# Performance work log

Hardware: AMD Instinct MI355X
Metric: run time of the kernel (lower is better)

The kernel has to match this reference:

```python
import jax, jax.numpy as jnp
import numpy as np

FIR_LO = {
    'db4': np.array([-0.0105974017850021, 0.0328830116668852, 0.0308413818355607, -0.1870348117188811,
                     -0.0279837694169839, 0.6308807679295904, 0.7148465705529155, 0.2303778133088964], np.float32),
    'db6': np.array([0.00107730108499558, -0.00477725751101065, -0.0005538422009938, 0.03158203931748603,
                     0.02752286553030533, -0.0975016055873225, -0.12976686756709563, 0.22626469396544,
                     0.3152503517092432, -0.7511339080210959, 0.4946238903984534, 0.1115407433501095], np.float32),
    'sym6': np.array([-0.007800708325034148, 0.001767711864242804, 0.04472490177066578, -0.02106029251230056,
                      -0.0726375227866, 0.3379294217282401, 0.787641141030194, 0.4910559419267466,
                      -0.048311742585632, -0.1179901111484105, 0.00349071208421747, 0.01540410932702737], np.float32),
    'coif5': np.array([-3.459977283621256e-05, -7.098330313814114e-05, 0.0004662169601128863, 0.001117518770890601,
                       -0.002574517688750223, -0.00900797613666158, 0.015880544863615904, 0.03455502757306163,
                       -0.08230192710688598, -0.07179982161931202, 0.42848347637761874, 0.7937772226256206,
                       0.4051769024096169, -0.06112339000267287, -0.06577191128185562, 0.023452696141836267,
                       0.007782596427325418, -0.003793512864491014, -0.0002606761356811993, 0.000107502882505652,
                       1.10319778524429e-05, -5.520763127949e-06, -1.0682196848076e-06, 5.236425333584e-07,
                       1.125098976034e-07, -5.417490769329e-08, -8.8631e-09, 4.2921e-09, 6.7e-10, -3.2e-10], np.float32),
}

CANDIDATES = ['db4', 'db6', 'sym6', 'coif5', 'bior53', 'bior97']
LIFT_53 = [(-0.5, True), (0.25, False)]
LIFT_97 = [(-1.586134342, True), (-0.05298011854, False), (0.8829110762, True), (0.4435068522, False)]


def _pad_reflect(x, hpad, wpad):
    if hpad == (0, 0) and wpad == (0, 0):
        return x
    return jnp.pad(x, ((0, 0), (0, 0), hpad, wpad), mode='reflect')


def _lo(name):
    lo = jnp.asarray(FIR_LO[name])
    return lo / (jnp.sqrt(jnp.sum(lo * lo)) + 1e-12)


def _hi_from_lo(lo):
    L = lo.shape[0]
    sign = jnp.cos(jnp.pi * jnp.arange(L, dtype=lo.dtype))  # (-1)^n
    return sign * lo[::-1]


def _sep_conv(x, k, dim):
    # x: (N,1,H,W); k: (L,) 1D filter applied separably along dim (cross-correlation, stride 1)
    L = k.shape[0]
    pl = (L - 1) // 2
    pa, pb = ((pl - 1, pl) if L % 2 == 0 else (pl, pl))
    if dim == 'W':
        xp = _pad_reflect(x, (0, 0), (pa, pb))
        kern = k.reshape(1, 1, 1, L)
    else:
        xp = _pad_reflect(x, (pa, pb), (0, 0))
        kern = k.reshape(1, 1, L, 1)
    return jax.lax.conv_general_dilated(xp, kern, (1, 1), 'VALID',
                                        dimension_numbers=('NCHW', 'OIHW', 'NCHW'))


def _split_even_odd(x, dim):
    if dim == 'W':
        if x.shape[3] % 2 == 1:
            x = _pad_reflect(x, (0, 0), (0, 1))
        return x[..., 0::2], x[..., 1::2]
    if x.shape[2] % 2 == 1:
        x = _pad_reflect(x, (0, 1), (0, 0))
    return x[..., 0::2, :], x[..., 1::2, :]


def _nb_sum(x, dim):
    # 0.5*(left+right) with reflect padding == conv with kernel [0.5, 0, 0.5]
    if dim == 'W':
        xp = _pad_reflect(x, (0, 0), (1, 1))
        return 0.5 * (xp[..., :-2] + xp[..., 2:])
    xp = _pad_reflect(x, (1, 1), (0, 0))
    return 0.5 * (xp[..., :-2, :] + xp[..., 2:, :])


def _lift(x, dim, steps, sA, sD):
    even, odd = _split_even_odd(x, dim)
    for coeff, is_pred in steps:
        if is_pred:
            odd = odd + coeff * _nb_sum(even, dim)
        else:
            even = even + coeff * _nb_sum(odd, dim)
    return sA * even, sD * odd


def _one_level_1d(x, cand, dim, p):
    if cand == 'bior53':
        return _lift(x, dim, LIFT_53, p['s53A'], p['s53D'])
    if cand == 'bior97':
        return _lift(x, dim, LIFT_97, p['s97A'], p['s97D'])
    lo = _lo(cand)
    return _sep_conv(x, lo, dim), _sep_conv(x, _hi_from_lo(lo), dim)


def _one_level_2d(x, cand, p):
    H, W = x.shape[2], x.shape[3]
    Lw, Hw = _one_level_1d(x, cand, 'W', p)
    LL, LH = _one_level_1d(Lw, cand, 'H', p)
    HL, HH = _one_level_1d(Hw, cand, 'H', p)

    def up(t):
        if t.shape[2] == H and t.shape[3] == W:
            return t
        return jax.image.resize(t, (t.shape[0], t.shape[1], H, W), method='bilinear')  # align_corners=False

    hf = p['hf']
    return up(LL), up(LH) * hf, up(HL) * hf, up(HH) * hf


def reference(x, gate_w1, gate_b1, gate_w2, gate_b2, scale53_A, scale53_D,
              scale97_A, scale97_D, hf_scale, proj_w, proj_b):
    B, C, H, W = x.shape
    # gate: 1x1 conv -> relu -> 1x1 conv -> softmax over K candidates
    h = jax.nn.relu(jnp.einsum('bchw,oc->bohw', x, gate_w1) + gate_b1[None, :, None, None])
    logits = jnp.einsum('bchw,oc->bohw', h, gate_w2) + gate_b2[None, :, None, None]
    gate_w = jax.nn.softmax(logits, axis=1)  # (B,K,H,W)

    x_bc = x.reshape(B * C, 1, H, W)
    p = {'s53A': scale53_A, 's53D': scale53_D, 's97A': scale97_A, 's97D': scale97_D, 'hf': hf_scale}
    bands = [_one_level_2d(x_bc, c, p) for c in CANDIDATES]
    # stack over K candidates -> (B*C, K, H, W) per subband
    LL = jnp.concatenate([b[0] for b in bands], axis=1)
    LH = jnp.concatenate([b[1] for b in bands], axis=1)
    HL = jnp.concatenate([b[2] for b in bands], axis=1)
    HH = jnp.concatenate([b[3] for b in bands], axis=1)

    w = jnp.repeat(gate_w, C, axis=0)  # (B*C,K,H,W), same as repeat_interleave on batch
    w = w / (jnp.sum(w, axis=1, keepdims=True) + 1e-12)
    LL_f = jnp.sum(LL * w, axis=1)
    LH_f = jnp.sum(LH * w, axis=1)
    HL_f = jnp.sum(HL * w, axis=1)
    HH_f = jnp.sum(HH * w, axis=1)

    Y = jnp.stack([LL_f, LH_f, HL_f, HH_f], axis=1).reshape(B, C * 4, H, W)
    return jnp.einsum('bchw,oc->bohw', Y, proj_w) + proj_b[None, :, None, None]


def setup_inputs() -> dict:
    key = jax.random.key(0)
    ks = jax.random.split(key, 5)
    C, hidden, K, Cout = 32, 8, 6, 32
    return {
        'x': jax.random.normal(ks[0], (4, C, 192, 192), jnp.float32),
        'gate_w1': jax.random.normal(ks[1], (hidden, C), jnp.float32) * (1.0 / np.sqrt(C)),
        'gate_b1': jnp.zeros((hidden,), jnp.float32),
        'gate_w2': jax.random.normal(ks[2], (K, hidden), jnp.float32) * (1.0 / np.sqrt(hidden)),
        'gate_b2': jnp.zeros((K,), jnp.float32),
        'scale53_A': jnp.float32(1.0),
        'scale53_D': jnp.float32(1.0),
        'scale97_A': jnp.float32(1.149604398),
        'scale97_D': jnp.float32(1.0 / 1.149604398),
        'hf_scale': jnp.float32(0.9),
        'proj_w': jax.random.normal(ks[3], (Cout, 4 * C), jnp.float32) * (1.0 / np.sqrt(4 * C)),
        'proj_b': jnp.zeros((Cout,), jnp.float32),
    }
```

## Files before the change

### kernel.cpp

```cpp
#include <hip/hip_runtime.h>
#include <hip/hip_fp16.h>

#define HW 36864
#define IMGS 128

typedef _Float16 h16;
typedef _Float16 v8h __attribute__((ext_vector_type(8)));
typedef _Float16 v4h __attribute__((ext_vector_type(4)));
typedef _Float16 v2h __attribute__((ext_vector_type(2)));
typedef float v4f __attribute__((ext_vector_type(4)));

static __device__ __forceinline__ int imax(int a, int b) { return a > b ? a : b; }
static __device__ __forceinline__ int imin(int a, int b) { return a < b ? a : b; }

__device__ __constant__ float LIFT_C[6] = {
  -0.5f, 0.25f,
  -1.586134342f, -0.05298011854f, 0.8829110762f, 0.4435068522f
};
__device__ __constant__ int FIR_L[4]   = {8, 12, 12, 30};
__device__ __constant__ int FIR_PA[4]  = {2, 4, 4, 13};
__device__ __constant__ int FIR_OFF[4] = {0, 8, 20, 32};

__device__ constexpr float FIRC[62] = {
  -0.0105974017850021f, 0.0328830116668852f, 0.0308413818355607f, -0.1870348117188811f,
  -0.0279837694169839f, 0.6308807679295904f, 0.7148465705529155f, 0.2303778133088964f,
  0.00107730108499558f, -0.00477725751101065f, -0.0005538422009938f, 0.03158203931748603f,
  0.02752286553030533f, -0.0975016055873225f, -0.12976686756709563f, 0.22626469396544f,
  0.3152503517092432f, -0.7511339080210959f, 0.4946238903984534f, 0.1115407433501095f,
  -0.007800708325034148f, 0.001767711864242804f, 0.04472490177066578f, -0.02106029251230056f,
  -0.0726375227866f, 0.3379294217282401f, 0.787641141030194f, 0.4910559419267466f,
  -0.048311742585632f, -0.1179901111484105f, 0.00349071208421747f, 0.01540410932702737f,
  -3.459977283621256e-05f, -7.098330313814114e-05f, 0.0004662169601128863f, 0.001117518770890601f,
  -0.002574517688750223f, -0.00900797613666158f, 0.015880544863615904f, 0.03455502757306163f,
  -0.08230192710688598f, -0.07179982161931202f, 0.42848347637761874f, 0.7937772226256206f,
  0.4051769024096169f, -0.06112339000267287f, -0.06577191128185562f, 0.023452696141836267f,
  0.007782596427325418f, -0.003793512864491014f, -0.0002606761356811993f, 0.000107502882505652f,
  1.10319778524429e-05f, -5.520763127949e-06f, -1.0682196848076e-06f, 5.236425333584e-07f,
  1.125098976034e-07f, -5.417490769329e-08f, -8.8631e-09f, 4.2921e-09f, 6.7e-10f, -3.2e-10f,
};

__global__ __launch_bounds__(256) void k_gate(
    const float* __restrict__ x, const float* __restrict__ w1, const float* __restrict__ b1,
    const float* __restrict__ w2, const float* __restrict__ b2, h16* __restrict__ gate)
{
  __shared__ float w1s[256], b1s[8], w2s[48], b2s[6];
  int tid = threadIdx.x;
  w1s[tid] = w1[tid];
  if (tid < 8)  b1s[tid] = b1[tid];
  if (tid < 48) w2s[tid] = w2[tid];
  if (tid < 6)  b2s[tid] = b2[tid];
  __syncthreads();
  int px = blockIdx.x * 256 + tid;
  int b = px / HW, p = px - b * HW;
  const float* xb = x + (size_t)b * 32 * HW + p;
  float xv[32];
#pragma unroll
  for (int c = 0; c < 32; ++c) xv[c] = xb[(size_t)c * HW];
  float hb[8];
#pragma unroll
  for (int j = 0; j < 8; ++j) {
    float s = b1s[j];
#pragma unroll
    for (int c = 0; c < 32; ++c) s += w1s[j * 32 + c] * xv[c];
    hb[j] = fmaxf(s, 0.f);
  }
  float e[6], mx = -1e30f;
#pragma unroll
  for (int k = 0; k < 6; ++k) {
    float s = b2s[k];
#pragma unroll
    for (int j = 0; j < 8; ++j) s += w2s[k * 8 + j] * hb[j];
    e[k] = s; mx = fmaxf(mx, s);
  }
  float se = 0.f;
#pragma unroll
  for (int k = 0; k < 6; ++k) { e[k] = expf(e[k] - mx); se += e[k]; }
  float inv = 1.f / se, s2 = 0.f;
#pragma unroll
  for (int k = 0; k < 6; ++k) { e[k] *= inv; s2 += e[k]; }
  float inv2 = 1.f / (s2 + 1e-12f);
  h16* gp = gate + (size_t)b * 6 * HW + p;
#pragma unroll
  for (int k = 0; k < 6; ++k) gp[(size_t)k * HW] = (h16)(e[k] * inv2);
}

__global__ __launch_bounds__(64) void k_build(
    h16* __restrict__ Kall, const float* __restrict__ s53A, const float* __restrict__ s53D,
    const float* __restrict__ s97A, const float* __restrict__ s97D)
{
  const int col = blockIdx.x;
  const int mat = blockIdx.y;
  const int cand = mat >> 1, side = mat & 1;
  const int tid = threadIdx.x;
  h16* out = Kall + (size_t)mat * HW;
  if (cand < 4) {
    const int Lf = FIR_L[cand], PA = FIR_PA[cand], OFF = FIR_OFF[cand];
    float ss = 0.f;
    for (int j = 0; j < Lf; ++j) ss += FIRC[OFF + j] * FIRC[OFF + j];
    const float invn = 1.f / (sqrtf(ss) + 1e-12f);
    for (int i = tid; i < 192; i += 64) {
      const int d = (i < 96) ? 1 : 2;
      const int q0 = i - d;
      const int i0 = imax(q0, 0), i1 = imin(q0 + 1, 189);
      const float tt = (float)d - (float)(2 * i + 1) * (1.f / 192.f);
      float c0 = 0.f, c1 = 0.f;
      for (int j = 0; j < Lf; ++j) {
        float fj = side ? (((j & 1) ? -1.f : 1.f) * FIRC[OFF + Lf - 1 - j]) : FIRC[OFF + j];
        fj *= invn;
        int r0 = i0 + j - PA; r0 = r0 < 0 ? -r0 : (r0 > 191 ? 382 - r0 : r0);
        int r1 = i1 + j - PA; r1 = r1 < 0 ? -r1 : (r1 > 191 ? 382 - r1 : r1);
        if (r0 == col) c0 += fj;
        if (r1 == col) c1 += fj;
      }
      out[(size_t)i * 192 + col] = (h16)((1.f - tt) * c0 + tt * c1);
    }
  } else {
    __shared__ float yb[192];
    __shared__ float sb[96];
    yb[tid] = 0.f; yb[tid + 64] = 0.f; yb[tid + 128] = 0.f;
    __syncthreads();
    if (tid == 0) yb[col] = 1.f;
    __syncthreads();
    const int c97 = (cand == 5);
    const int base = c97 ? 2 : 0, ns = c97 ? 4 : 2;
    for (int s = 0; s < ns; ++s) {
      const float cf = LIFT_C[base + s] * 0.5f;
      for (int j = tid; j < 96; j += 64) {
        int jm = (j == 0) ? 1 : j - 1, jp = (j == 95) ? 94 : j + 1;
        if ((s & 1) == 0) yb[2 * j + 1] += cf * (yb[2 * jm] + yb[2 * jp]);
        else              yb[2 * j]     += cf * (yb[2 * jm + 1] + yb[2 * jp + 1]);
      }
      __syncthreads();
    }
    const float sA = c97 ? s97A[0] : s53A[0];
    const float sD = c97 ? s97D[0] : s53D[0];
    for (int u = tid; u < 96; u += 64)
      sb[u] = side ? sD * yb[2 * u + 1] : sA * yb[2 * u];
    __syncthreads();
    for (int i = tid; i < 192; i += 64) {
      const int u0 = (i >> 1) + (i & 1) - 1;
      const float tt = (i & 1) ? 0.25f : 0.75f;
      const int a0 = imax(u0, 0), a1 = imin(u0 + 1, 95);
      out[(size_t)i * 192 + col] = (h16)((1.f - tt) * sb[a0] + tt * sb[a1]);
    }
  }
}

__global__ __launch_bounds__(768) void k_gw(
    const float* __restrict__ x, const h16* __restrict__ Kall, h16* __restrict__ P)
{
  __shared__ h16 As[96 * 200];
  const int half = blockIdx.x;
  const int img  = blockIdx.y;
  const int tid = threadIdx.x;
  const float* xi = x + (size_t)img * HW + (size_t)half * 96 * 192;
  for (int u = tid; u < 2304; u += 768) {
    int r = u / 24, c8 = u - r * 24;
    float4 v0 = *(const float4*)(xi + (size_t)r * 192 + c8 * 8);
    float4 v1 = *(const float4*)(xi + (size_t)r * 192 + c8 * 8 + 4);
    v8h h;
    h[0] = (h16)v0.x; h[1] = (h16)v0.y; h[2] = (h16)v0.z; h[3] = (h16)v0.w;
    h[4] = (h16)v1.x; h[5] = (h16)v1.y; h[6] = (h16)v1.z; h[7] = (h16)v1.w;
    *(v8h*)(As + (size_t)r * 200 + c8 * 8) = h;
  }
  __syncthreads();
  const int lane = tid & 63, wv = tid >> 6;
  const int lm = lane & 15, quad = lane >> 4;
  const int mt = wv >> 1, nh = wv & 1;
  const int mrow = mt * 16;
  const int hg = half * 96 + mrow + quad * 4;
  for (int plane = 0; plane < 12; ++plane) {
    const h16* KB = Kall + (size_t)plane * HW;
    h16* Pp = P + ((size_t)plane * IMGS + img) * HW;
    for (int t6 = 0; t6 < 6; ++t6) {
      const int nt = nh * 6 + t6;
      const int n0 = nt * 16;
      const int ktlo = imax(0, (n0 - 24) >> 5), kthi = imin(5, (n0 + 39) >> 5);
      v4f C = (v4f){0.f, 0.f, 0.f, 0.f};
      for (int kt = ktlo; kt <= kthi; ++kt) {
        const int k0 = kt * 32 + quad * 8;
        v8h a = *(const v8h*)(As + (size_t)(mrow + lm) * 200 + k0);
        v8h b = *(const v8h*)(KB + (size_t)(n0 + lm) * 192 + k0);
        C = __builtin_amdgcn_mfma_f32_16x16x32_f16(a, b, C, 0, 0, 0);
      }
      const int q = n0 / 48;
      const int wq = n0 - q * 48 + lm;
      v4h o;
      o[0] = (h16)C[0]; o[1] = (h16)C[1]; o[2] = (h16)C[2]; o[3] = (h16)C[3];
      *(v4h*)(Pp + (size_t)q * 9216 + (size_t)wq * 192 + hg) = o;
    }
  }
}

__global__ __launch_bounds__(512, 2) void k_gh2(
    const h16* __restrict__ Kall, const h16* __restrict__ P, const h16* __restrict__ gate,
    const float* __restrict__ hfp, h16* __restrict__ sf)
{
  __shared__ h16 Bs[2][48 * 200];
  const int bx = blockIdx.x;
  const int sw = bx & 1, qt = bx >> 1;
  const int img = blockIdx.y;
  const int bimg = img >> 5;
  const int tid = threadIdx.x;
  const int lane = tid & 63, wv = tid >> 6;
  const int lm = lane & 15, quad = lane >> 4;
  const int sh = wv & 1, w4 = wv >> 1;
  const int w0q = qt * 48;

  const int wp0 = tid / 24,          c80 = tid - wp0 * 24;
  const int it1 = tid + 512;
  const int wp1 = it1 / 24,          c81 = it1 - wp1 * 24;
  const int it2 = tid + 1024;
  const int wp2 = it2 / 24,          c82 = it2 - wp2 * 24;

  v4f acc[3][3];
#pragma unroll
  for (int mi = 0; mi < 3; ++mi)
#pragma unroll
    for (int nt = 0; nt < 3; ++nt) acc[mi][nt] = (v4f){0.f, 0.f, 0.f, 0.f};

  const h16* Ps = P + ((size_t)sw * IMGS + img) * HW + (size_t)qt * 9216;
  v8h p0 = *(const v8h*)(Ps + (size_t)wp0 * 192 + c80 * 8);
  v8h p1 = *(const v8h*)(Ps + (size_t)wp1 * 192 + c81 * 8);
  v8h p2;
  if (tid < 128) p2 = *(const v8h*)(Ps + (size_t)wp2 * 192 + c82 * 8);

  int cur = 0;
  for (int cand = 0; cand < 6; ++cand) {
    h16* B = Bs[cur];
    *(v8h*)(B + (size_t)wp0 * 200 + c80 * 8) = p0;
    *(v8h*)(B + (size_t)wp1 * 200 + c81 * 8) = p1;
    if (tid < 128) *(v8h*)(B + (size_t)wp2 * 200 + c82 * 8) = p2;
    __syncthreads();
    if (cand < 5) {
      const h16* Pn = P + ((size_t)((cand + 1) * 2 + sw) * IMGS + img) * HW + (size_t)qt * 9216;
      p0 = *(const v8h*)(Pn + (size_t)wp0 * 192 + c80 * 8);
      p1 = *(const v8h*)(Pn + (size_t)wp1 * 192 + c81 * 8);
      if (tid < 128) p2 = *(const v8h*)(Pn + (size_t)wp2 * 192 + c82 * 8);
    }
    const h16* g16 = gate + (size_t)(bimg * 6 + cand) * HW;
    const h16* KB = Kall + (size_t)(cand * 2 + sh) * HW;
#pragma unroll
    for (int mi = 0; mi < 3; ++mi) {
      const int m0 = w4 * 48 + mi * 16;
      const int ktlo = imax(0, (m0 - 24) >> 5), kthi = imin(5, (m0 + 39) >> 5);
      const int hr0 = m0 + quad * 4;
      float g[3][4];
#pragma unroll
      for (int nt = 0; nt < 3; ++nt)
#pragma unroll
        for (int r = 0; r < 4; ++r)
          g[nt][r] = (float)g16[(size_t)(hr0 + r) * 192 + w0q + nt * 16 + lm];
      v4f C[3];
#pragma unroll
      for (int nt = 0; nt < 3; ++nt) C[nt] = (v4f){0.f, 0.f, 0.f, 0.f};
      for (int kt = ktlo; kt <= kthi; ++kt) {
        const int k0 = kt * 32 + quad * 8;
        v8h a = *(const v8h*)(KB + (size_t)(m0 + lm) * 192 + k0);
#pragma unroll
        for (int nt = 0; nt < 3; ++nt) {
          v8h b = *(const v8h*)(B + (size_t)(nt * 16 + lm) * 200 + k0);
          C[nt] = __builtin_amdgcn_mfma_f32_16x16x32_f16(a, b, C[nt], 0, 0, 0);
        }
      }
#pragma unroll
      for (int nt = 0; nt < 3; ++nt)
#pragma unroll
        for (int r = 0; r < 4; ++r)
          acc[mi][nt][r] += g[nt][r] * C[nt][r];
    }
    cur ^= 1;
  }
  const float hfv = hfp[0];
  const int s = sw * 2 + sh;
  const float f = (s == 0) ? 1.f : hfv;
  h16* Op = sf + ((size_t)img * 4 + s) * HW;
#pragma unroll
  for (int mi = 0; mi < 3; ++mi) {
    const int hr0 = w4 * 48 + mi * 16 + quad * 4;
#pragma unroll
    for (int nt = 0; nt < 3; ++nt) {
      const int wc = w0q + nt * 16 + lm;
#pragma unroll
      for (int r = 0; r < 4; ++r)
        Op[(size_t)(hr0 + r) * 192 + wc] = (h16)(f * acc[mi][nt][r]);
    }
  }
}

__global__ __launch_bounds__(256) void k_proj(
    const h16* __restrict__ sf, const float* __restrict__ pw,
    const float* __restrict__ pb, float* __restrict__ out)
{
  const int tid = threadIdx.x;
  const int lane = tid & 63;
  const int og = __builtin_amdgcn_readfirstlane(tid >> 6);
  const int b = blockIdx.x / 288;
  const int p = (blockIdx.x - b * 288) * 128 + lane * 2;
  const h16* sfb = sf + (size_t)(b * 128) * HW + p;
  const float* pwb = pw + og * 8 * 128;
  float acc0[8], acc1[8];
#pragma unroll
  for (int oo = 0; oo < 8; ++oo) { acc0[oo] = 0.f; acc1[oo] = 0.f; }
#pragma unroll 4
  for (int ch = 0; ch < 128; ++ch) {
    v2h hv = *(const v2h*)(sfb + (size_t)ch * HW);
    const float v0 = (float)hv[0], v1 = (float)hv[1];
#pragma unroll
    for (int oo = 0; oo < 8; ++oo) {
      const float w = pwb[oo * 128 + ch];
      acc0[oo] = fmaf(w, v0, acc0[oo]);
      acc1[oo] = fmaf(w, v1, acc1[oo]);
    }
  }
#pragma unroll
  for (int oo = 0; oo < 8; ++oo) {
    float2 o2;
    o2.x = acc0[oo] + pb[og * 8 + oo];
    o2.y = acc1[oo] + pb[og * 8 + oo];
    *(float2*)(out + (size_t)(b * 32 + og * 8 + oo) * HW + p) = o2;
  }
}

extern "C" void kernel_launch(void* const* d_in, const int* in_sizes, int n_in,
                              void* d_out, int out_size, void* d_ws, size_t ws_size,
                              hipStream_t stream) {
  (void)in_sizes; (void)n_in; (void)out_size; (void)ws_size;
  const float* x    = (const float*)d_in[0];
  const float* gw1  = (const float*)d_in[1];
  const float* gb1  = (const float*)d_in[2];
  const float* gw2  = (const float*)d_in[3];
  const float* gb2  = (const float*)d_in[4];
  const float* s53A = (const float*)d_in[5];
  const float* s53D = (const float*)d_in[6];
  const float* s97A = (const float*)d_in[7];
  const float* s97D = (const float*)d_in[8];
  const float* hfp  = (const float*)d_in[9];
  const float* pw   = (const float*)d_in[10];
  const float* pb   = (const float*)d_in[11];
  float* out = (float*)d_out;

  h16* gate = (h16*)d_ws;
  h16* Kall = (h16*)((char*)d_ws + 1769472);
  h16* P    = (h16*)((char*)d_ws + 2654208);
  h16* sf   = (h16*)((char*)d_ws + 115900416);

  hipLaunchKernelGGL(k_gate, dim3(576), dim3(256), 0, stream, x, gw1, gb1, gw2, gb2, gate);
  hipLaunchKernelGGL(k_build, dim3(192, 12), dim3(64), 0, stream, Kall, s53A, s53D, s97A, s97D);
  hipLaunchKernelGGL(k_gw, dim3(2, IMGS), dim3(768), 0, stream, x, Kall, P);
  hipLaunchKernelGGL(k_gh2, dim3(8, IMGS), dim3(512), 0, stream, Kall, P, gate, hfp, sf);
  hipLaunchKernelGGL(k_proj, dim3(1152), dim3(256), 0, stream, sf, pw, pb, out);
}
```

Measured before the change: 305.8 us.

## Split gw planes across blocks, transpose gate, drop LDS staging in gh2

k_gw now launches four times as many blocks, each handling 3 of the 12 planes, and declares a min-occupancy of 2 blocks. This adds parallelism at the cost of reloading and converting the x tile once per plane group. The gate tensor is written transposed so k_gh2 can read it as 4-wide vectors instead of scattered scalars. k_gh2 drops its double-buffered LDS staging of P and reads B fragments straight from global memory, and both GEMM loops become fixed 3-step unrolled K windows. The risk is more global and cache traffic in k_gh2 in exchange for no LDS use and no barriers.

```diff
diff --git a/kernel.cpp b/kernel.cpp
--- a/kernel.cpp
+++ b/kernel.cpp
@@ -79,7 +79,8 @@
 #pragma unroll
   for (int k = 0; k < 6; ++k) { e[k] *= inv; s2 += e[k]; }
   float inv2 = 1.f / (s2 + 1e-12f);
-  h16* gp = gate + (size_t)b * 6 * HW + p;
+  const int h = p / 192, w = p - h * 192;
+  h16* gp = gate + (size_t)b * 6 * HW + (size_t)w * 192 + h;
 #pragma unroll
   for (int k = 0; k < 6; ++k) gp[(size_t)k * HW] = (h16)(e[k] * inv2);
 }
@@ -146,11 +147,11 @@
   }
 }
 
-__global__ __launch_bounds__(768) void k_gw(
+__global__ __launch_bounds__(768, 2) void k_gw(
     const float* __restrict__ x, const h16* __restrict__ Kall, h16* __restrict__ P)
 {
   __shared__ h16 As[96 * 200];
-  const int half = blockIdx.x;
+  const int half = blockIdx.x & 1, pg = blockIdx.x >> 1;
   const int img  = blockIdx.y;
   const int tid = threadIdx.x;
   const float* xi = x + (size_t)img * HW + (size_t)half * 96 * 192;
@@ -169,16 +170,19 @@
   const int mt = wv >> 1, nh = wv & 1;
   const int mrow = mt * 16;
   const int hg = half * 96 + mrow + quad * 4;
-  for (int plane = 0; plane < 12; ++plane) {
+#pragma unroll
+  for (int pl = 0; pl < 3; ++pl) {
+    const int plane = pg * 3 + pl;
     const h16* KB = Kall + (size_t)plane * HW;
     h16* Pp = P + ((size_t)plane * IMGS + img) * HW;
+#pragma unroll
     for (int t6 = 0; t6 < 6; ++t6) {
-      const int nt = nh * 6 + t6;
-      const int n0 = nt * 16;
-      const int ktlo = imax(0, (n0 - 24) >> 5), kthi = imin(5, (n0 + 39) >> 5);
+      const int n0 = (nh * 6 + t6) * 16;
+      int kt0 = (n0 - 24) >> 5; kt0 = kt0 < 0 ? 0 : (kt0 > 3 ? 3 : kt0);
       v4f C = (v4f){0.f, 0.f, 0.f, 0.f};
-      for (int kt = ktlo; kt <= kthi; ++kt) {
-        const int k0 = kt * 32 + quad * 8;
+#pragma unroll
+      for (int kt = 0; kt < 3; ++kt) {
+        const int k0 = (kt0 + kt) * 32 + quad * 8;
         v8h a = *(const v8h*)(As + (size_t)(mrow + lm) * 200 + k0);
         v8h b = *(const v8h*)(KB + (size_t)(n0 + lm) * 192 + k0);
         C = __builtin_amdgcn_mfma_f32_16x16x32_f16(a, b, C, 0, 0, 0);
@@ -193,10 +197,9 @@
 }
 
 __global__ __launch_bounds__(512, 2) void k_gh2(
-    const h16* __restrict__ Kall, const h16* __restrict__ P, const h16* __restrict__ gate,
+    const h16* __restrict__ Kall, const h16* __restrict__ P, const h16* __restrict__ gate_t,
     const float* __restrict__ hfp, h16* __restrict__ sf)
 {
-  __shared__ h16 Bs[2][48 * 200];
   const int bx = blockIdx.x;
   const int sw = bx & 1, qt = bx >> 1;
   const int img = blockIdx.y;
@@ -207,59 +210,38 @@
   const int sh = wv & 1, w4 = wv >> 1;
   const int w0q = qt * 48;
 
-  const int wp0 = tid / 24,          c80 = tid - wp0 * 24;
-  const int it1 = tid + 512;
-  const int wp1 = it1 / 24,          c81 = it1 - wp1 * 24;
-  const int it2 = tid + 1024;
-  const int wp2 = it2 / 24,          c82 = it2 - wp2 * 24;
-
   v4f acc[3][3];
 #pragma unroll
   for (int mi = 0; mi < 3; ++mi)
 #pragma unroll
     for (int nt = 0; nt < 3; ++nt) acc[mi][nt] = (v4f){0.f, 0.f, 0.f, 0.f};
 
-  const h16* Ps = P + ((size_t)sw * IMGS + img) * HW + (size_t)qt * 9216;
-  v8h p0 = *(const v8h*)(Ps + (size_t)wp0 * 192 + c80 * 8);
-  v8h p1 = *(const v8h*)(Ps + (size_t)wp1 * 192 + c81 * 8);
-  v8h p2;
-  if (tid < 128) p2 = *(const v8h*)(Ps + (size_t)wp2 * 192 + c82 * 8);
-
-  int cur = 0;
   for (int cand = 0; cand < 6; ++cand) {
-    h16* B = Bs[cur];
-    *(v8h*)(B + (size_t)wp0 * 200 + c80 * 8) = p0;
-    *(v8h*)(B + (size_t)wp1 * 200 + c81 * 8) = p1;
-    if (tid < 128) *(v8h*)(B + (size_t)wp2 * 200 + c82 * 8) = p2;
-    __syncthreads();
-    if (cand < 5) {
-      const h16* Pn = P + ((size_t)((cand + 1) * 2 + sw) * IMGS + img) * HW + (size_t)qt * 9216;
-      p0 = *(const v8h*)(Pn + (size_t)wp0 * 192 + c80 * 8);
-      p1 = *(const v8h*)(Pn + (size_t)wp1 * 192 + c81 * 8);
-      if (tid < 128) p2 = *(const v8h*)(Pn + (size_t)wp2 * 192 + c82 * 8);
-    }
-    const h16* g16 = gate + (size_t)(bimg * 6 + cand) * HW;
+    const h16* Pp = P + ((size_t)(cand * 2 + sw) * IMGS + img) * HW + (size_t)qt * 9216;
     const h16* KB = Kall + (size_t)(cand * 2 + sh) * HW;
+    const h16* gt = gate_t + (size_t)(bimg * 6 + cand) * HW;
 #pragma unroll
     for (int mi = 0; mi < 3; ++mi) {
       const int m0 = w4 * 48 + mi * 16;
-      const int ktlo = imax(0, (m0 - 24) >> 5), kthi = imin(5, (m0 + 39) >> 5);
+      int kt0 = (m0 - 24) >> 5; kt0 = kt0 < 0 ? 0 : (kt0 > 3 ? 3 : kt0);
       const int hr0 = m0 + quad * 4;
       float g[3][4];
 #pragma unroll
-      for (int nt = 0; nt < 3; ++nt)
-#pragma unroll
-        for (int r = 0; r < 4; ++r)
-          g[nt][r] = (float)g16[(size_t)(hr0 + r) * 192 + w0q + nt * 16 + lm];
+      for (int nt = 0; nt < 3; ++nt) {
+        v4h gv = *(const v4h*)(gt + (size_t)(w0q + nt * 16 + lm) * 192 + hr0);
+#pragma unroll
+        for (int r = 0; r < 4; ++r) g[nt][r] = (float)gv[r];
+      }
       v4f C[3];
 #pragma unroll
       for (int nt = 0; nt < 3; ++nt) C[nt] = (v4f){0.f, 0.f, 0.f, 0.f};
-      for (int kt = ktlo; kt <= kthi; ++kt) {
-        const int k0 = kt * 32 + quad * 8;
+#pragma unroll
+      for (int kt = 0; kt < 3; ++kt) {
+        const int k0 = (kt0 + kt) * 32 + quad * 8;
         v8h a = *(const v8h*)(KB + (size_t)(m0 + lm) * 192 + k0);
 #pragma unroll
         for (int nt = 0; nt < 3; ++nt) {
-          v8h b = *(const v8h*)(B + (size_t)(nt * 16 + lm) * 200 + k0);
+          v8h b = *(const v8h*)(Pp + (size_t)(nt * 16 + lm) * 192 + k0);
           C[nt] = __builtin_amdgcn_mfma_f32_16x16x32_f16(a, b, C[nt], 0, 0, 0);
         }
       }
@@ -269,7 +251,6 @@
         for (int r = 0; r < 4; ++r)
           acc[mi][nt][r] += g[nt][r] * C[nt][r];
     }
-    cur ^= 1;
   }
   const float hfv = hfp[0];
   const int s = sw * 2 + sh;
@@ -347,7 +328,7 @@
 
   hipLaunchKernelGGL(k_gate, dim3(576), dim3(256), 0, stream, x, gw1, gb1, gw2, gb2, gate);
   hipLaunchKernelGGL(k_build, dim3(192, 12), dim3(64), 0, stream, Kall, s53A, s53D, s97A, s97D);
-  hipLaunchKernelGGL(k_gw, dim3(2, IMGS), dim3(768), 0, stream, x, Kall, P);
+  hipLaunchKernelGGL(k_gw, dim3(8, IMGS), dim3(768), 0, stream, x, Kall, P);
   hipLaunchKernelGGL(k_gh2, dim3(8, IMGS), dim3(512), 0, stream, Kall, P, gate, hfp, sf);
   hipLaunchKernelGGL(k_proj, dim3(1152), dim3(256), 0, stream, sf, pw, pb, out);
 }
```

Measured after the change: 463.4 us. 51.6% more time.
